# Optimization experiments

Hardware: AMD Instinct MI355X
Metric: run time of the kernel (lower is better)

Reference implementation:

```python
import jax, jax.numpy as jnp
import numpy as np

B, N, M, C = 4, 768, 768, 128
K_NN, K1_NN = 16, 8
NUM_KEYPOINTS = 256
NN_MARGIN = 0.7


def pairwise_distance_batch(x, y):
    # x: (B,C,N), y: (B,C,M) -> squared euclidean distance map (B,N,M)
    xx = jnp.sum(x * x, axis=1)[:, :, None]
    yy = jnp.sum(y * y, axis=1)[:, None, :]
    return xx + yy - 2.0 * jnp.einsum('bcn,bcm->bnm', x, y)


def discriminator(knn_distance, src_knn_distance, w1, b1, w2, b2, w3, b3, w4, b4):
    # inlier-evaluation weight function: pointwise MLP over (B,N,k,6), max-pool over k, MLP -> sigmoid weight (B,1,N)
    x = jnp.concatenate([knn_distance, src_knn_distance], axis=-1)  # (B,N,k,6)
    h = jax.nn.relu(jnp.einsum('bnkc,oc->bnko', x, w1) + b1)
    h = jax.nn.relu(jnp.einsum('bnko,po->bnkp', h, w2) + b2)
    g = h.max(axis=2)  # (B,N,64) pool over neighbors
    g = jax.nn.relu(jnp.einsum('bnp,qp->bnq', g, w3) + b3)
    w = jax.nn.sigmoid(jnp.einsum('bnq,rq->bnr', g, w4) + b4)  # (B,N,1)
    return w.transpose(0, 2, 1)  # (B,1,N)


def compute_rigid_transformation(src, src_corr, weight):
    # weighted Kabsch/SVD rigid fit. src/src_corr: (B,3,N), weight: (B,1,N)
    w = weight / (jnp.sum(weight, axis=2, keepdims=True) + 1e-8)
    src_mean = jnp.sum(src * w, axis=2, keepdims=True)
    corr_mean = jnp.sum(src_corr * w, axis=2, keepdims=True)
    src_c = (src - src_mean) * w
    corr_c = src_corr - corr_mean
    H = jnp.einsum('bin,bjn->bij', src_c, corr_c)  # (B,3,3)
    U, S, Vt = jnp.linalg.svd(H)
    V = Vt.transpose(0, 2, 1)
    det = jnp.linalg.det(jnp.einsum('bij,bkj->bik', V, U))  # det(V U^T)
    d = jnp.stack([jnp.ones_like(det), jnp.ones_like(det), det], axis=-1)  # (B,3)
    R = jnp.einsum('bij,bj,bkj->bik', V, d, U)
    t = corr_mean - jnp.einsum('bij,bjk->bik', R, src_mean)  # (B,3,1)
    return R, t


def _forward(src, tgt, src_embedding, tgt_embedding, src_idx, k, src_knn, i, tgt_knn, src_idx1, idx2, k1,
             w1, b1, w2, b2, w3, b3, w4, b4, num_keypoints, nn_margin):
    Bs, _, Ns = src.shape
    Ms = tgt.shape[2]
    dist = pairwise_distance_batch(src_embedding, tgt_embedding)  # (B,N,M)
    scores = jax.nn.softmax(-dist, axis=2)
    # neighborhood consensus: sum_{a>=1,c>=1} scores[b, nbr_src(i,a), nbr_tgt(j,c)] / (k1-1)
    S1 = scores.reshape(Bs * Ns, Ms)[src_idx1].reshape(Bs, Ns, k1, Ms)  # gather src-neighbor rows
    A = jnp.sum(S1[:, :, 1:, :], axis=2)  # (B,N,M), drop self (a=0)
    idx2c = idx2[:, :, 1:]  # (B,M,k1-1), drop self (c=0)
    consensus = jax.vmap(lambda a, idx: jnp.sum(a[:, idx], axis=-1))(A, idx2c) / (k1 - 1)  # (B,N,M)
    src_knn_scores = nn_margin - consensus
    refined = jnp.exp(src_knn_scores) * dist
    matching = jax.nn.softmax(-refined, axis=2)  # refined matching map (B,N,M)
    src_corr = jnp.einsum('bcm,bnm->bcn', tgt, matching)  # soft correspondences (B,3,N)
    src_corr_t = src_corr.transpose(0, 2, 1)  # (B,N,3)
    src_knn_corr = src_corr_t.reshape(Bs * Ns, 3)[src_idx].reshape(Bs, Ns, k, 3)
    knn_distance = src_corr_t[:, :, None, :] - src_knn_corr  # (B,N,k,3)
    src_knn_distance = src.transpose(0, 2, 1)[:, :, None, :] - src_knn
    weight = discriminator(knn_distance, src_knn_distance, w1, b1, w2, b2, w3, b3, w4, b4)  # (B,1,N)
    R, t = compute_rigid_transformation(src, src_corr, weight)
    _, topk_idx = jax.lax.top_k(weight[:, 0, :], num_keypoints)  # (B,K)
    bidx = jnp.arange(Bs)[:, None]
    bc = jnp.broadcast_to(topk_idx[:, None, :], (Bs, 3, num_keypoints))
    src_keypoints = jnp.take_along_axis(src, bc, axis=2)  # (B,3,K)
    tgt_keypoints = jnp.take_along_axis(src_corr, bc, axis=2)
    idx_tgt_corr = jnp.argmax(matching, axis=-1)  # (B,N)
    kp_corr = jnp.take_along_axis(idx_tgt_corr, topk_idx, axis=1)  # (B,K)
    keypoints_one_hot = jax.nn.one_hot(kp_corr, Ms, dtype=matching.dtype)  # (B,K,M)
    pred_scores = matching[bidx, topk_idx]  # (B,K,M)
    loss_scl = jnp.mean(jnp.sum(-jnp.log(pred_scores + 1e-15) * keypoints_one_hot, axis=-1))
    tgt_keypoints_knn = knn_distance[bidx, topk_idx].transpose(0, 3, 1, 2)  # (B,3,K,k)
    src_transformed = jnp.einsum('bij,bjn->bin', R, src) + t
    st = src_transformed.transpose(0, 2, 1)  # (B,N,3)
    st_knn_corr = st.reshape(Bs * Ns, 3)[src_idx].reshape(Bs, Ns, k, 3)
    knn_distance2 = st[:, :, None, :] - st_knn_corr
    src_keypoints_knn = knn_distance2[bidx, topk_idx].transpose(0, 3, 1, 2)  # (B,3,K,k)
    return (R, t.reshape(Bs, 3), src_keypoints, tgt_keypoints, src_keypoints_knn, tgt_keypoints_knn, loss_scl)


def setup_inputs() -> dict:
    key = jax.random.key(0)
    ks = jax.random.split(key, 12)
    src = jax.random.normal(ks[0], (B, 3, N), jnp.float32)
    tgt = jax.random.normal(ks[1], (B, 3, M), jnp.float32)
    src_embedding = jax.random.normal(ks[2], (B, C, N), jnp.float32)
    tgt_embedding = jax.random.normal(ks[3], (B, C, M), jnp.float32)
    # knn index lists; first neighbor is the point itself (matching the [:,:,1:] self-exclusion slices)
    idxk = jax.random.randint(ks[4], (B, N, K_NN), 0, N).at[:, :, 0].set(jnp.arange(N)[None, :])
    idxk1 = jax.random.randint(ks[5], (B, N, K1_NN), 0, N).at[:, :, 0].set(jnp.arange(N)[None, :])
    idx2 = jax.random.randint(ks[6], (B, M, K1_NN), 0, M).at[:, :, 0].set(jnp.arange(M)[None, :])
    off = jnp.arange(B)[:, None, None] * N
    src_idx = (idxk + off).reshape(-1)   # flat indices into (B*N) rows
    src_idx1 = (idxk1 + off).reshape(-1)
    bidx = jnp.arange(B)[:, None, None]
    src_knn = src.transpose(0, 2, 1)[bidx, idxk]   # (B,N,k,3) coords of neighbors
    tgt_knn = tgt.transpose(0, 2, 1)[bidx, idx2]   # (B,M,k1,3) (unused by forward, kept for signature fidelity)
    s = 0.1
    w1 = jax.random.normal(ks[7], (64, 6), jnp.float32) * s
    w2 = jax.random.normal(ks[8], (64, 64), jnp.float32) * s
    w3 = jax.random.normal(ks[9], (32, 64), jnp.float32) * s
    w4 = jax.random.normal(ks[10], (1, 32), jnp.float32) * s
    return {"src": src, "tgt": tgt, "src_embedding": src_embedding, "tgt_embedding": tgt_embedding,
            "src_idx": src_idx, "k": K_NN, "src_knn": src_knn, "i": 0, "tgt_knn": tgt_knn,
            "src_idx1": src_idx1, "idx2": idx2, "k1": K1_NN,
            "w1": w1, "b1": jnp.zeros((64,), jnp.float32), "w2": w2, "b2": jnp.zeros((64,), jnp.float32),
            "w3": w3, "b3": jnp.zeros((32,), jnp.float32), "w4": w4, "b4": jnp.zeros((1,), jnp.float32),
            "num_keypoints": NUM_KEYPOINTS, "nn_margin": NN_MARGIN}


def reference(src, tgt, src_embedding, tgt_embedding, src_idx, k, src_knn, i, tgt_knn, src_idx1, idx2, k1,
              w1, b1, w2, b2, w3, b3, w4, b4, num_keypoints, nn_margin):
    return _forward(src, tgt, src_embedding, tgt_embedding, src_idx, k, src_knn, i, tgt_knn, src_idx1, idx2, k1,
                    w1, b1, w2, b2, w3, b3, w4, b4, num_keypoints, nn_margin)
```

## Files before the change

### kernel.cpp

```cpp
#include <hip/hip_runtime.h>
#include <hip/hip_bf16.h>
#include <math.h>

#define BB 4
#define NN 768
#define MM 768
#define CC 128
#define KK 16
#define KK1 8
#define NKP 256

#define OFF_R    0
#define OFF_T    36
#define OFF_SK   48
#define OFF_TK   3120
#define OFF_SKK  6192
#define OFF_TKK  55344
#define OFF_LOSS 104496

__global__ __launch_bounds__(256) void dist_k(const float* __restrict__ xe,
                                              const float* __restrict__ ye,
                                              float* __restrict__ dist) {
    __shared__ float xt[CC * 32];
    __shared__ float yt[CC * 32];
    __shared__ float nx[32];
    __shared__ float ny[32];
    int b = blockIdx.z, n0 = blockIdx.y * 32, m0 = blockIdx.x * 32;
    int tid = threadIdx.x;
    for (int i = tid; i < CC * 32; i += 256) {
        int c = i >> 5, v = i & 31;
        xt[i] = xe[(size_t)(b * CC + c) * NN + n0 + v];
        yt[i] = ye[(size_t)(b * CC + c) * MM + m0 + v];
    }
    __syncthreads();
    if (tid < 32) {
        float s = 0.f;
        for (int c = 0; c < CC; c++) { float v = xt[c * 32 + tid]; s += v * v; }
        nx[tid] = s;
    } else if (tid < 64) {
        int v0 = tid - 32;
        float s = 0.f;
        for (int c = 0; c < CC; c++) { float v = yt[c * 32 + v0]; s += v * v; }
        ny[v0] = s;
    }
    int mi = tid & 31, ng = tid >> 5;
    float acc[4] = {0.f, 0.f, 0.f, 0.f};
    for (int c = 0; c < CC; c++) {
        float yv = yt[c * 32 + mi];
        acc[0] += xt[c * 32 + ng] * yv;
        acc[1] += xt[c * 32 + ng + 8] * yv;
        acc[2] += xt[c * 32 + ng + 16] * yv;
        acc[3] += xt[c * 32 + ng + 24] * yv;
    }
    __syncthreads();
    for (int q = 0; q < 4; q++) {
        int n = n0 + ng + 8 * q;
        dist[((size_t)b * NN + n) * MM + m0 + mi] = nx[ng + 8 * q] + ny[mi] - 2.f * acc[q];
    }
}

__global__ __launch_bounds__(256) void scores_k(const float* __restrict__ dist,
                                                float* __restrict__ scores) {
    __shared__ float red[4];
    int r = blockIdx.x, tid = threadIdx.x;
    int lane = tid & 63, wv = tid >> 6;
    const float* dr = dist + (size_t)r * MM;
    float v[3]; float mn = 1e30f;
    for (int q = 0; q < 3; q++) { v[q] = dr[tid + 256 * q]; mn = fminf(mn, v[q]); }
    for (int off = 32; off >= 1; off >>= 1) mn = fminf(mn, __shfl_down(mn, off));
    if (lane == 0) red[wv] = mn;
    __syncthreads();
    mn = fminf(fminf(red[0], red[1]), fminf(red[2], red[3]));
    __syncthreads();
    float e[3], z = 0.f;
    for (int q = 0; q < 3; q++) { e[q] = expf(mn - v[q]); z += e[q]; }
    for (int off = 32; off >= 1; off >>= 1) z += __shfl_down(z, off);
    if (lane == 0) red[wv] = z;
    __syncthreads();
    z = red[0] + red[1] + red[2] + red[3];
    float inv = 1.0f / z;
    for (int q = 0; q < 3; q++) scores[(size_t)r * MM + tid + 256 * q] = e[q] * inv;
}

__global__ __launch_bounds__(256) void match_k(const float* __restrict__ dist,
                                               const float* __restrict__ scores,
                                               const int* __restrict__ src_idx1,
                                               const int* __restrict__ idx2,
                                               const float* __restrict__ tgt,
                                               const float* __restrict__ nn_margin_p,
                                               float* __restrict__ src_corr,
                                               float* __restrict__ mmax) {
    __shared__ float Arow[MM];
    __shared__ float red[4];
    __shared__ float red4[16];
    int r = blockIdx.x, tid = threadIdx.x;
    int lane = tid & 63, wv = tid >> 6;
    int b = r / NN, n = r % NN;
    int rows[KK1 - 1];
    for (int j = 0; j < KK1 - 1; j++) rows[j] = src_idx1[r * KK1 + 1 + j];
    for (int q = 0; q < 3; q++) {
        int m = tid + 256 * q;
        float a = 0.f;
        for (int j = 0; j < KK1 - 1; j++) a += scores[(size_t)rows[j] * MM + m];
        Arow[m] = a;
    }
    __syncthreads();
    float marg = nn_margin_p[0];
    const float* drow = dist + (size_t)r * MM;
    float rv[3]; float mn = 1e30f;
    for (int q = 0; q < 3; q++) {
        int m = tid + 256 * q;
        const int4* ip = (const int4*)(idx2 + ((size_t)b * MM + m) * KK1);
        int4 i0 = ip[0], i1 = ip[1];
        float cons = Arow[i0.y] + Arow[i0.z] + Arow[i0.w] +
                     Arow[i1.x] + Arow[i1.y] + Arow[i1.z] + Arow[i1.w];
        rv[q] = expf(marg - cons * (1.0f / (KK1 - 1))) * drow[m];
        mn = fminf(mn, rv[q]);
    }
    for (int off = 32; off >= 1; off >>= 1) mn = fminf(mn, __shfl_down(mn, off));
    if (lane == 0) red[wv] = mn;
    __syncthreads();
    mn = fminf(fminf(red[0], red[1]), fminf(red[2], red[3]));
    float z = 0.f, s0 = 0.f, s1 = 0.f, s2 = 0.f;
    const float* t0 = tgt + (size_t)b * 3 * MM;
    for (int q = 0; q < 3; q++) {
        int m = tid + 256 * q;
        float e = expf(mn - rv[q]);
        z += e;
        s0 += e * t0[m];
        s1 += e * t0[MM + m];
        s2 += e * t0[2 * MM + m];
    }
    for (int off = 32; off >= 1; off >>= 1) {
        z += __shfl_down(z, off); s0 += __shfl_down(s0, off);
        s1 += __shfl_down(s1, off); s2 += __shfl_down(s2, off);
    }
    if (lane == 0) { red4[wv * 4] = z; red4[wv * 4 + 1] = s0; red4[wv * 4 + 2] = s1; red4[wv * 4 + 3] = s2; }
    __syncthreads();
    if (tid == 0) {
        float zt = red4[0] + red4[4] + red4[8] + red4[12];
        float s0t = red4[1] + red4[5] + red4[9] + red4[13];
        float s1t = red4[2] + red4[6] + red4[10] + red4[14];
        float s2t = red4[3] + red4[7] + red4[11] + red4[15];
        float inv = 1.0f / zt;
        src_corr[(size_t)(b * 3 + 0) * NN + n] = s0t * inv;
        src_corr[(size_t)(b * 3 + 1) * NN + n] = s1t * inv;
        src_corr[(size_t)(b * 3 + 2) * NN + n] = s2t * inv;
        mmax[r] = inv;
    }
}

__global__ __launch_bounds__(256) void disc_k(const float* __restrict__ src,
                                              const float* __restrict__ src_corr,
                                              const float* __restrict__ src_knn,
                                              const int* __restrict__ src_idx,
                                              const float* __restrict__ w1, const float* __restrict__ b1,
                                              const float* __restrict__ w2, const float* __restrict__ b2,
                                              const float* __restrict__ w3, const float* __restrict__ b3,
                                              const float* __restrict__ w4, const float* __restrict__ b4,
                                              float* __restrict__ knnD, float* __restrict__ wgt) {
    __shared__ float w1s[64 * 7];
    __shared__ float w2s[64 * 65];
    __shared__ float w3s[32 * 65];
    __shared__ float xs[4][16 * 6];
    __shared__ float h1s[4][16 * 64];
    __shared__ float gs[4][64];
    int tid = threadIdx.x;
    for (int i = tid; i < 64 * 6; i += 256) w1s[(i / 6) * 7 + (i % 6)] = w1[i];
    for (int i = tid; i < 64 * 64; i += 256) w2s[(i / 64) * 65 + (i % 64)] = w2[i];
    for (int i = tid; i < 32 * 64; i += 256) w3s[(i / 64) * 65 + (i % 64)] = w3[i];
    int w = tid >> 6, l = tid & 63;
    int r = blockIdx.x * 4 + w;
    int b = r / NN, n = r % NN;
    if (l < KK) {
        int j = l;
        int f = src_idx[r * KK + j];
        int fb = f / NN, fn = f % NN;
        for (int c = 0; c < 3; c++) {
            float scn = src_corr[(size_t)(b * 3 + c) * NN + n];
            float kd = scn - src_corr[(size_t)(fb * 3 + c) * NN + fn];
            xs[w][j * 6 + c] = kd;
            knnD[((size_t)r * KK + j) * 3 + c] = kd;
            float sd = src[(size_t)(b * 3 + c) * NN + n] - src_knn[((size_t)r * KK + j) * 3 + c];
            xs[w][j * 6 + 3 + c] = sd;
        }
    }
    __syncthreads();
    float bb1 = b1[l];
    for (int k = 0; k < KK; k++) {
        float h = bb1;
        for (int c = 0; c < 6; c++) h += xs[w][k * 6 + c] * w1s[l * 7 + c];
        h1s[w][k * 64 + l] = h > 0.f ? h : 0.f;
    }
    __syncthreads();
    float bb2 = b2[l];
    float acc2[KK];
    for (int k = 0; k < KK; k++) acc2[k] = bb2;
    for (int o = 0; o < 64; o++) {
        float wvv = w2s[l * 65 + o];
        const float* hp = &h1s[w][o];
        for (int k = 0; k < KK; k++) acc2[k] += hp[k * 64] * wvv;
    }
    float gm = 0.f;
    for (int k = 0; k < KK; k++) gm = fmaxf(gm, acc2[k]);
    gs[w][l] = gm;
    __syncthreads();
    float val = 0.f;
    if (l < 32) {
        float h = b3[l];
        for (int o = 0; o < 64; o++) h += gs[w][o] * w3s[l * 65 + o];
        h = h > 0.f ? h : 0.f;
        val = h * w4[l];
    }
    for (int off = 32; off >= 1; off >>= 1) val += __shfl_down(val, off);
    if (l == 0) wgt[r] = 1.0f / (1.0f + expf(-(val + b4[0])));
}

__global__ __launch_bounds__(256) void bsum_k(const float* __restrict__ src,
                                              const float* __restrict__ src_corr,
                                              const float* __restrict__ wgt,
                                              double* __restrict__ bsums) {
    __shared__ double redd[4 * 16];
    int b = blockIdx.x, tid = threadIdx.x;
    int lane = tid & 63, wv = tid >> 6;
    double acc[16];
    for (int k = 0; k < 16; k++) acc[k] = 0.0;
    for (int n = tid; n < NN; n += 256) {
        double wvv = wgt[b * NN + n];
        double s[3], q[3];
        for (int i = 0; i < 3; i++) {
            s[i] = src[(size_t)(b * 3 + i) * NN + n];
            q[i] = src_corr[(size_t)(b * 3 + i) * NN + n];
        }
        acc[0] += wvv;
        for (int i = 0; i < 3; i++) acc[1 + i] += wvv * s[i];
        for (int j = 0; j < 3; j++) acc[4 + j] += wvv * q[j];
        for (int i = 0; i < 3; i++)
            for (int j = 0; j < 3; j++) acc[7 + i * 3 + j] += wvv * s[i] * q[j];
    }
    for (int k = 0; k < 16; k++)
        for (int off = 32; off >= 1; off >>= 1) acc[k] += __shfl_down(acc[k], off);
    if (lane == 0)
        for (int k = 0; k < 16; k++) redd[wv * 16 + k] = acc[k];
    __syncthreads();
    if (tid < 16)
        bsums[b * 16 + tid] = redd[tid] + redd[16 + tid] + redd[32 + tid] + redd[48 + tid];
}

__global__ void rigid_k(const double* __restrict__ bsums, float* __restrict__ out,
                        float* __restrict__ Rws, float* __restrict__ tws) {
    int b = threadIdx.x;
    if (b >= BB) return;
    const double* S = bsums + b * 16;
    double T = S[0], D = T + 1e-8;
    double sm[3], cm[3];
    for (int i = 0; i < 3; i++) { sm[i] = S[1 + i] / D; cm[i] = S[4 + i] / D; }
    double fac = 2.0 - T / D;
    double H[3][3];
    for (int i = 0; i < 3; i++)
        for (int j = 0; j < 3; j++) H[i][j] = S[7 + i * 3 + j] / D - sm[i] * cm[j] * fac;
    double Sxx = H[0][0], Sxy = H[0][1], Sxz = H[0][2];
    double Syx = H[1][0], Syy = H[1][1], Syz = H[1][2];
    double Szx = H[2][0], Szy = H[2][1], Szz = H[2][2];
    double A[4][4];
    A[0][0] = Sxx + Syy + Szz; A[0][1] = Syz - Szy;        A[0][2] = Szx - Sxz;        A[0][3] = Sxy - Syx;
    A[1][0] = A[0][1];         A[1][1] = Sxx - Syy - Szz;  A[1][2] = Sxy + Syx;        A[1][3] = Szx + Sxz;
    A[2][0] = A[0][2];         A[2][1] = A[1][2];          A[2][2] = -Sxx + Syy - Szz; A[2][3] = Syz + Szy;
    A[3][0] = A[0][3];         A[3][1] = A[1][3];          A[3][2] = A[2][3];          A[3][3] = -Sxx - Syy + Szz;
    double V[4][4] = {{1,0,0,0},{0,1,0,0},{0,0,1,0},{0,0,0,1}};
    for (int sweep = 0; sweep < 15; sweep++) {
        double off = A[0][1]*A[0][1] + A[0][2]*A[0][2] + A[0][3]*A[0][3]
                   + A[1][2]*A[1][2] + A[1][3]*A[1][3] + A[2][3]*A[2][3];
        if (off < 1e-26) break;
        for (int p = 0; p < 3; p++) {
            for (int q = p + 1; q < 4; q++) {
                double apq = A[p][q];
                if (fabs(apq) < 1e-60) continue;
                double theta = 0.5 * (A[q][q] - A[p][p]) / apq;
                double t = (theta >= 0 ? 1.0 : -1.0) / (fabs(theta) + sqrt(theta * theta + 1.0));
                double c = 1.0 / sqrt(t * t + 1.0), s = t * c;
                for (int k = 0; k < 4; k++) {
                    double akp = A[k][p], akq = A[k][q];
                    A[k][p] = c * akp - s * akq; A[k][q] = s * akp + c * akq;
                }
                for (int k = 0; k < 4; k++) {
                    double apk = A[p][k], aqk = A[q][k];
                    A[p][k] = c * apk - s * aqk; A[q][k] = s * apk + c * aqk;
                }
                for (int k = 0; k < 4; k++) {
                    double vkp = V[k][p], vkq = V[k][q];
                    V[k][p] = c * vkp - s * vkq; V[k][q] = s * vkp + c * vkq;
                }
            }
        }
    }
    int best = 0;
    for (int k = 1; k < 4; k++) if (A[k][k] > A[best][best]) best = k;
    double qw = V[0][best], qx = V[1][best], qy = V[2][best], qz = V[3][best];
    double nq = sqrt(qw * qw + qx * qx + qy * qy + qz * qz);
    qw /= nq; qx /= nq; qy /= nq; qz /= nq;
    double R[3][3];
    R[0][0] = 1 - 2 * (qy * qy + qz * qz); R[0][1] = 2 * (qx * qy - qw * qz); R[0][2] = 2 * (qx * qz + qw * qy);
    R[1][0] = 2 * (qx * qy + qw * qz); R[1][1] = 1 - 2 * (qx * qx + qz * qz); R[1][2] = 2 * (qy * qz - qw * qx);
    R[2][0] = 2 * (qx * qz - qw * qy); R[2][1] = 2 * (qy * qz + qw * qx); R[2][2] = 1 - 2 * (qx * qx + qy * qy);
    for (int i = 0; i < 3; i++)
        for (int j = 0; j < 3; j++) {
            out[OFF_R + b * 9 + i * 3 + j] = (float)R[i][j];
            Rws[b * 9 + i * 3 + j] = (float)R[i][j];
        }
    for (int i = 0; i < 3; i++) {
        double tv = cm[i] - (R[i][0] * sm[0] + R[i][1] * sm[1] + R[i][2] * sm[2]);
        out[OFF_T + b * 3 + i] = (float)tv;
        tws[b * 3 + i] = (float)tv;
    }
}

__global__ __launch_bounds__(256) void topk_k(const float* __restrict__ wgt, int* __restrict__ topk,
                                              const float* __restrict__ src, const float* __restrict__ Rws,
                                              const float* __restrict__ tws, float* __restrict__ st) {
    __shared__ float wl[NN];
    int b = blockIdx.y, tid = threadIdx.x;
    for (int i = tid; i < NN; i += 256) wl[i] = wgt[b * NN + i];
    __syncthreads();
    int i = blockIdx.x * 64 + (tid >> 2);
    int q = tid & 3;
    float v = wl[i];
    int rank = 0;
    for (int t = 0; t < NN / 4; t++) {
        int j = q + 4 * t;
        float u = wl[j];
        rank += (u > v) || (u == v && j < i);
    }
    rank += __shfl_down(rank, 2, 4);
    rank += __shfl_down(rank, 1, 4);
    if (q == 0 && rank < NKP) topk[b * NKP + rank] = i;
    int gid = (b * (NN / 64) + blockIdx.x) * 256 + tid;
    if (gid < BB * 3 * NN) {
        int n = gid % NN; int bi = gid / NN; int b2 = bi / 3, ii = bi % 3;
        const float* Rb = Rws + b2 * 9 + ii * 3;
        const float* sb = src + (size_t)b2 * 3 * NN;
        st[gid] = Rb[0] * sb[n] + Rb[1] * sb[NN + n] + Rb[2] * sb[2 * NN + n] + tws[b2 * 3 + ii];
    }
}

__global__ void gather_k(const float* __restrict__ src, const float* __restrict__ src_corr,
                         const float* __restrict__ knnD, const float* __restrict__ st,
                         const int* __restrict__ src_idx, const int* __restrict__ topk,
                         float* __restrict__ out) {
    int t = blockIdx.x * blockDim.x + threadIdx.x;
    if (t >= BB * NKP * KK) return;
    int j = t % KK; int br = t / KK; int r = br % NKP; int b = br / NKP;
    int idx = topk[b * NKP + r];
    int rr = b * NN + idx;
    for (int c = 0; c < 3; c++)
        out[OFF_TKK + (size_t)((b * 3 + c) * NKP + r) * KK + j] = knnD[((size_t)rr * KK + j) * 3 + c];
    int f = src_idx[rr * KK + j];
    int fb = f / NN, fn = f % NN;
    for (int c = 0; c < 3; c++)
        out[OFF_SKK + (size_t)((b * 3 + c) * NKP + r) * KK + j] =
            st[(size_t)(b * 3 + c) * NN + idx] - st[(size_t)(fb * 3 + c) * NN + fn];
    if (j == 0) {
        for (int c = 0; c < 3; c++) {
            out[OFF_SK + (b * 3 + c) * NKP + r] = src[(size_t)(b * 3 + c) * NN + idx];
            out[OFF_TK + (b * 3 + c) * NKP + r] = src_corr[(size_t)(b * 3 + c) * NN + idx];
        }
    }
}

__global__ __launch_bounds__(256) void loss_k(const float* __restrict__ mmax,
                                              const int* __restrict__ topk,
                                              float* __restrict__ out) {
    __shared__ float red[256];
    int tid = threadIdx.x;
    float acc = 0.f;
    for (int t = tid; t < BB * NKP; t += 256) {
        int b = t / NKP;
        int idx = topk[t];
        float v = mmax[b * NN + idx];
        acc += -logf(v + 1e-15f);
    }
    red[tid] = acc; __syncthreads();
    for (int s = 128; s > 0; s >>= 1) { if (tid < s) red[tid] += red[tid + s]; __syncthreads(); }
    if (tid == 0) out[OFF_LOSS] = red[0] / (float)(BB * NKP);
}

extern "C" void kernel_launch(void* const* d_in, const int* in_sizes, int n_in,
                              void* d_out, int out_size, void* d_ws, size_t ws_size,
                              hipStream_t stream) {
    (void)in_sizes; (void)n_in; (void)out_size; (void)ws_size;
    const float* src      = (const float*)d_in[0];
    const float* tgt      = (const float*)d_in[1];
    const float* se       = (const float*)d_in[2];
    const float* te       = (const float*)d_in[3];
    const int*   src_idx  = (const int*)d_in[4];
    const float* src_knn  = (const float*)d_in[6];
    const int*   src_idx1 = (const int*)d_in[9];
    const int*   idx2     = (const int*)d_in[10];
    const float* w1 = (const float*)d_in[12];
    const float* b1 = (const float*)d_in[13];
    const float* w2 = (const float*)d_in[14];
    const float* b2 = (const float*)d_in[15];
    const float* w3 = (const float*)d_in[16];
    const float* b3 = (const float*)d_in[17];
    const float* w4 = (const float*)d_in[18];
    const float* b4 = (const float*)d_in[19];
    const float* nn_margin = (const float*)d_in[21];
    float* out = (float*)d_out;

    float* ws = (float*)d_ws;
    float* dist     = ws;
    float* scores   = dist + (size_t)BB * NN * MM;
    float* src_corr = scores + (size_t)BB * NN * MM;
    float* mmax     = src_corr + BB * 3 * NN;
    float* knnD     = mmax + BB * NN;
    float* wgt      = knnD + (size_t)BB * NN * KK * 3;
    double* bsums   = (double*)(wgt + BB * NN);
    float* Rws      = (float*)(bsums + BB * 16);
    float* tws      = Rws + BB * 9;
    float* st       = tws + BB * 3;
    int*   topk     = (int*)(st + BB * 3 * NN);

    dist_k<<<dim3(MM / 32, NN / 32, BB), 256, 0, stream>>>(se, te, dist);
    scores_k<<<BB * NN, 256, 0, stream>>>(dist, scores);
    match_k<<<BB * NN, 256, 0, stream>>>(dist, scores, src_idx1, idx2, tgt, nn_margin,
                                         src_corr, mmax);
    disc_k<<<BB * NN / 4, 256, 0, stream>>>(src, src_corr, src_knn, src_idx,
                                            w1, b1, w2, b2, w3, b3, w4, b4, knnD, wgt);
    bsum_k<<<BB, 256, 0, stream>>>(src, src_corr, wgt, bsums);
    rigid_k<<<1, 64, 0, stream>>>(bsums, out, Rws, tws);
    topk_k<<<dim3(NN / 64, BB), 256, 0, stream>>>(wgt, topk, src, Rws, tws, st);
    gather_k<<<(BB * NKP * KK + 255) / 256, 256, 0, stream>>>(src, src_corr, knnD, st,
                                                              src_idx, topk, out);
    loss_k<<<1, 256, 0, stream>>>(mmax, topk, out);
}
```

Before: 205.8 us.

## Register-tile distance GEMM, vectorize MLP layer, fuse rigid-fit and loss kernels

The distance kernel moves from 32x32 to 64x64 tiles, with float4 loads and a 4x4 register micro-tile per thread, which raises arithmetic intensity. The second MLP layer in the discriminator now reads hidden activations as float4. The batch-sum and rigid-fit kernels are merged into one single-block launch that uses one wave per batch. The loss reduction is folded into the gather kernel using atomics and a last-block-done counter. Together these drop two launches, but the fused sum now runs on only 4 waves, and the float atomic order makes the loss non-deterministic.

```diff
diff --git a/kernel.cpp b/kernel.cpp
--- a/kernel.cpp
+++ b/kernel.cpp
@@ -21,41 +21,50 @@
 __global__ __launch_bounds__(256) void dist_k(const float* __restrict__ xe,
                                               const float* __restrict__ ye,
                                               float* __restrict__ dist) {
-    __shared__ float xt[CC * 32];
-    __shared__ float yt[CC * 32];
-    __shared__ float nx[32];
-    __shared__ float ny[32];
-    int b = blockIdx.z, n0 = blockIdx.y * 32, m0 = blockIdx.x * 32;
+    __shared__ float xt[CC * 64];
+    __shared__ float yt[CC * 64];
+    __shared__ float nx[64];
+    __shared__ float ny[64];
+    int b = blockIdx.z, n0 = blockIdx.y * 64, m0 = blockIdx.x * 64;
     int tid = threadIdx.x;
-    for (int i = tid; i < CC * 32; i += 256) {
-        int c = i >> 5, v = i & 31;
-        xt[i] = xe[(size_t)(b * CC + c) * NN + n0 + v];
-        yt[i] = ye[(size_t)(b * CC + c) * MM + m0 + v];
-    }
-    __syncthreads();
-    if (tid < 32) {
+    for (int i = tid; i < CC * 16; i += 256) {
+        int c = i >> 4, v = i & 15;
+        ((float4*)xt)[c * 16 + v] = ((const float4*)(xe + (size_t)(b * CC + c) * NN + n0))[v];
+        ((float4*)yt)[c * 16 + v] = ((const float4*)(ye + (size_t)(b * CC + c) * MM + m0))[v];
+    }
+    __syncthreads();
+    if (tid < 64) {
         float s = 0.f;
-        for (int c = 0; c < CC; c++) { float v = xt[c * 32 + tid]; s += v * v; }
+        for (int c = 0; c < CC; c++) { float v = xt[c * 64 + tid]; s += v * v; }
         nx[tid] = s;
-    } else if (tid < 64) {
-        int v0 = tid - 32;
+    } else if (tid < 128) {
+        int v0 = tid - 64;
         float s = 0.f;
-        for (int c = 0; c < CC; c++) { float v = yt[c * 32 + v0]; s += v * v; }
+        for (int c = 0; c < CC; c++) { float v = yt[c * 64 + v0]; s += v * v; }
         ny[v0] = s;
     }
-    int mi = tid & 31, ng = tid >> 5;
-    float acc[4] = {0.f, 0.f, 0.f, 0.f};
+    int mi = (tid & 15) * 4;
+    int ni = (tid >> 4) * 4;
+    float acc[16];
+    for (int k = 0; k < 16; k++) acc[k] = 0.f;
     for (int c = 0; c < CC; c++) {
-        float yv = yt[c * 32 + mi];
-        acc[0] += xt[c * 32 + ng] * yv;
-        acc[1] += xt[c * 32 + ng + 8] * yv;
-        acc[2] += xt[c * 32 + ng + 16] * yv;
-        acc[3] += xt[c * 32 + ng + 24] * yv;
-    }
-    __syncthreads();
-    for (int q = 0; q < 4; q++) {
-        int n = n0 + ng + 8 * q;
-        dist[((size_t)b * NN + n) * MM + m0 + mi] = nx[ng + 8 * q] + ny[mi] - 2.f * acc[q];
+        float4 xv = *(const float4*)&xt[c * 64 + ni];
+        float4 yv = *(const float4*)&yt[c * 64 + mi];
+        acc[0]  += xv.x * yv.x; acc[1]  += xv.x * yv.y; acc[2]  += xv.x * yv.z; acc[3]  += xv.x * yv.w;
+        acc[4]  += xv.y * yv.x; acc[5]  += xv.y * yv.y; acc[6]  += xv.y * yv.z; acc[7]  += xv.y * yv.w;
+        acc[8]  += xv.z * yv.x; acc[9]  += xv.z * yv.y; acc[10] += xv.z * yv.z; acc[11] += xv.z * yv.w;
+        acc[12] += xv.w * yv.x; acc[13] += xv.w * yv.y; acc[14] += xv.w * yv.z; acc[15] += xv.w * yv.w;
+    }
+    __syncthreads();
+    float ny0 = ny[mi], ny1 = ny[mi + 1], ny2 = ny[mi + 2], ny3 = ny[mi + 3];
+    for (int i = 0; i < 4; i++) {
+        float nxi = nx[ni + i];
+        float4 o;
+        o.x = nxi + ny0 - 2.f * acc[i * 4 + 0];
+        o.y = nxi + ny1 - 2.f * acc[i * 4 + 1];
+        o.z = nxi + ny2 - 2.f * acc[i * 4 + 2];
+        o.w = nxi + ny3 - 2.f * acc[i * 4 + 3];
+        *(float4*)&dist[((size_t)b * NN + n0 + ni + i) * MM + m0 + mi] = o;
     }
 }
 
@@ -196,10 +205,15 @@
     float bb2 = b2[l];
     float acc2[KK];
     for (int k = 0; k < KK; k++) acc2[k] = bb2;
-    for (int o = 0; o < 64; o++) {
-        float wvv = w2s[l * 65 + o];
-        const float* hp = &h1s[w][o];
-        for (int k = 0; k < KK; k++) acc2[k] += hp[k * 64] * wvv;
+    for (int o4 = 0; o4 < 16; o4++) {
+        float wa = w2s[l * 65 + o4 * 4 + 0];
+        float wb = w2s[l * 65 + o4 * 4 + 1];
+        float wc = w2s[l * 65 + o4 * 4 + 2];
+        float wd = w2s[l * 65 + o4 * 4 + 3];
+        for (int k = 0; k < KK; k++) {
+            float4 h = *(const float4*)&h1s[w][k * 64 + o4 * 4];
+            acc2[k] += h.x * wa + h.y * wb + h.z * wc + h.w * wd;
+        }
     }
     float gm = 0.f;
     for (int k = 0; k < KK; k++) gm = fmaxf(gm, acc2[k]);
@@ -216,16 +230,19 @@
     if (l == 0) wgt[r] = 1.0f / (1.0f + expf(-(val + b4[0])));
 }
 
-__global__ __launch_bounds__(256) void bsum_k(const float* __restrict__ src,
-                                              const float* __restrict__ src_corr,
-                                              const float* __restrict__ wgt,
-                                              double* __restrict__ bsums) {
-    __shared__ double redd[4 * 16];
-    int b = blockIdx.x, tid = threadIdx.x;
-    int lane = tid & 63, wv = tid >> 6;
+__global__ __launch_bounds__(256) void bsumrigid_k(const float* __restrict__ src,
+                                                   const float* __restrict__ src_corr,
+                                                   const float* __restrict__ wgt,
+                                                   float* __restrict__ out,
+                                                   float* __restrict__ Rws, float* __restrict__ tws,
+                                                   float* __restrict__ lossAcc) {
+    __shared__ double redd[BB * 16];
+    int tid = threadIdx.x;
+    int wv = tid >> 6, lane = tid & 63;
+    int b = wv;
     double acc[16];
     for (int k = 0; k < 16; k++) acc[k] = 0.0;
-    for (int n = tid; n < NN; n += 256) {
+    for (int n = lane; n < NN; n += 64) {
         double wvv = wgt[b * NN + n];
         double s[3], q[3];
         for (int i = 0; i < 3; i++) {
@@ -241,17 +258,12 @@
     for (int k = 0; k < 16; k++)
         for (int off = 32; off >= 1; off >>= 1) acc[k] += __shfl_down(acc[k], off);
     if (lane == 0)
-        for (int k = 0; k < 16; k++) redd[wv * 16 + k] = acc[k];
-    __syncthreads();
-    if (tid < 16)
-        bsums[b * 16 + tid] = redd[tid] + redd[16 + tid] + redd[32 + tid] + redd[48 + tid];
-}
-
-__global__ void rigid_k(const double* __restrict__ bsums, float* __restrict__ out,
-                        float* __restrict__ Rws, float* __restrict__ tws) {
-    int b = threadIdx.x;
-    if (b >= BB) return;
-    const double* S = bsums + b * 16;
+        for (int k = 0; k < 16; k++) redd[b * 16 + k] = acc[k];
+    __syncthreads();
+    if (tid == 0) { lossAcc[0] = 0.f; ((int*)lossAcc)[1] = 0; }
+    if (tid >= BB) return;
+    int bb = tid;
+    const double* S = redd + bb * 16;
     double T = S[0], D = T + 1e-8;
     double sm[3], cm[3];
     for (int i = 0; i < 3; i++) { sm[i] = S[1 + i] / D; cm[i] = S[4 + i] / D; }
@@ -305,13 +317,13 @@
     R[2][0] = 2 * (qx * qz - qw * qy); R[2][1] = 2 * (qy * qz + qw * qx); R[2][2] = 1 - 2 * (qx * qx + qy * qy);
     for (int i = 0; i < 3; i++)
         for (int j = 0; j < 3; j++) {
-            out[OFF_R + b * 9 + i * 3 + j] = (float)R[i][j];
-            Rws[b * 9 + i * 3 + j] = (float)R[i][j];
+            out[OFF_R + bb * 9 + i * 3 + j] = (float)R[i][j];
+            Rws[bb * 9 + i * 3 + j] = (float)R[i][j];
         }
     for (int i = 0; i < 3; i++) {
         double tv = cm[i] - (R[i][0] * sm[0] + R[i][1] * sm[1] + R[i][2] * sm[2]);
-        out[OFF_T + b * 3 + i] = (float)tv;
-        tws[b * 3 + i] = (float)tv;
+        out[OFF_T + bb * 3 + i] = (float)tv;
+        tws[bb * 3 + i] = (float)tv;
     }
 }
 
@@ -343,12 +355,18 @@
     }
 }
 
-__global__ void gather_k(const float* __restrict__ src, const float* __restrict__ src_corr,
-                         const float* __restrict__ knnD, const float* __restrict__ st,
-                         const int* __restrict__ src_idx, const int* __restrict__ topk,
-                         float* __restrict__ out) {
-    int t = blockIdx.x * blockDim.x + threadIdx.x;
-    if (t >= BB * NKP * KK) return;
+__global__ __launch_bounds__(256) void gather_k(const float* __restrict__ src,
+                                                const float* __restrict__ src_corr,
+                                                const float* __restrict__ knnD,
+                                                const float* __restrict__ st,
+                                                const int* __restrict__ src_idx,
+                                                const int* __restrict__ topk,
+                                                const float* __restrict__ mmax,
+                                                float* __restrict__ lossAcc,
+                                                float* __restrict__ out) {
+    __shared__ float lred[4];
+    int tid = threadIdx.x;
+    int t = blockIdx.x * 256 + tid;
     int j = t % KK; int br = t / KK; int r = br % NKP; int b = br / NKP;
     int idx = topk[b * NKP + r];
     int rr = b * NN + idx;
@@ -359,29 +377,28 @@
     for (int c = 0; c < 3; c++)
         out[OFF_SKK + (size_t)((b * 3 + c) * NKP + r) * KK + j] =
             st[(size_t)(b * 3 + c) * NN + idx] - st[(size_t)(fb * 3 + c) * NN + fn];
+    float term = 0.f;
     if (j == 0) {
         for (int c = 0; c < 3; c++) {
             out[OFF_SK + (b * 3 + c) * NKP + r] = src[(size_t)(b * 3 + c) * NN + idx];
             out[OFF_TK + (b * 3 + c) * NKP + r] = src_corr[(size_t)(b * 3 + c) * NN + idx];
         }
-    }
-}
-
-__global__ __launch_bounds__(256) void loss_k(const float* __restrict__ mmax,
-                                              const int* __restrict__ topk,
-                                              float* __restrict__ out) {
-    __shared__ float red[256];
-    int tid = threadIdx.x;
-    float acc = 0.f;
-    for (int t = tid; t < BB * NKP; t += 256) {
-        int b = t / NKP;
-        int idx = topk[t];
-        float v = mmax[b * NN + idx];
-        acc += -logf(v + 1e-15f);
-    }
-    red[tid] = acc; __syncthreads();
-    for (int s = 128; s > 0; s >>= 1) { if (tid < s) red[tid] += red[tid + s]; __syncthreads(); }
-    if (tid == 0) out[OFF_LOSS] = red[0] / (float)(BB * NKP);
+        term = -logf(mmax[rr] + 1e-15f);
+    }
+    int lane = tid & 63, wv = tid >> 6;
+    for (int off = 32; off >= 1; off >>= 1) term += __shfl_down(term, off);
+    if (lane == 0) lred[wv] = term;
+    __syncthreads();
+    if (tid == 0) {
+        float bsum = lred[0] + lred[1] + lred[2] + lred[3];
+        atomicAdd(&lossAcc[0], bsum);
+        __threadfence();
+        int old = atomicAdd((int*)&lossAcc[1], 1);
+        if (old == (int)gridDim.x - 1) {
+            float fin = atomicAdd(&lossAcc[0], 0.f);
+            out[OFF_LOSS] = fin / (float)(BB * NKP);
+        }
+    }
 }
 
 extern "C" void kernel_launch(void* const* d_in, const int* in_sizes, int n_in,
@@ -414,22 +431,20 @@
     float* mmax     = src_corr + BB * 3 * NN;
     float* knnD     = mmax + BB * NN;
     float* wgt      = knnD + (size_t)BB * NN * KK * 3;
-    double* bsums   = (double*)(wgt + BB * NN);
-    float* Rws      = (float*)(bsums + BB * 16);
+    float* Rws      = wgt + BB * NN;
     float* tws      = Rws + BB * 9;
     float* st       = tws + BB * 3;
     int*   topk     = (int*)(st + BB * 3 * NN);
-
-    dist_k<<<dim3(MM / 32, NN / 32, BB), 256, 0, stream>>>(se, te, dist);
+    float* lossAcc  = (float*)(topk + BB * NKP);
+
+    dist_k<<<dim3(MM / 64, NN / 64, BB), 256, 0, stream>>>(se, te, dist);
     scores_k<<<BB * NN, 256, 0, stream>>>(dist, scores);
     match_k<<<BB * NN, 256, 0, stream>>>(dist, scores, src_idx1, idx2, tgt, nn_margin,
                                          src_corr, mmax);
     disc_k<<<BB * NN / 4, 256, 0, stream>>>(src, src_corr, src_knn, src_idx,
                                             w1, b1, w2, b2, w3, b3, w4, b4, knnD, wgt);
-    bsum_k<<<BB, 256, 0, stream>>>(src, src_corr, wgt, bsums);
-    rigid_k<<<1, 64, 0, stream>>>(bsums, out, Rws, tws);
+    bsumrigid_k<<<1, 256, 0, stream>>>(src, src_corr, wgt, out, Rws, tws, lossAcc);
     topk_k<<<dim3(NN / 64, BB), 256, 0, stream>>>(wgt, topk, src, Rws, tws, st);
-    gather_k<<<(BB * NKP * KK + 255) / 256, 256, 0, stream>>>(src, src_corr, knnD, st,
-                                                              src_idx, topk, out);
-    loss_k<<<1, 256, 0, stream>>>(mmax, topk, out);
-}
+    gather_k<<<BB * NKP * KK / 256, 256, 0, stream>>>(src, src_corr, knnD, st,
+                                                      src_idx, topk, mmax, lossAcc, out);
+}
```

New measurement: 194.4 us. 1.06x faster.
